# Performance work log

Hardware: AMD Instinct MI355X
Metric: run time of the kernel (lower is better)

The kernel has to match this reference:

```python
import jax, jax.numpy as jnp
import numpy as np

H = 1024
HEADS = 16
FFN = 4096
EPS = 1e-5


def _layernorm(x, g, b):
    mu = jnp.mean(x, axis=-1, keepdims=True)
    var = jnp.mean((x - mu) ** 2, axis=-1, keepdims=True)
    return (x - mu) * jax.lax.rsqrt(var + EPS) * g + b


def setup_inputs() -> dict:
    key = jax.random.key(0)
    ks = jax.random.split(key, 12)
    N, L = 2, 2048
    s = 1.0 / np.sqrt(H)
    inp = {
        "src_hidden": jax.random.normal(ks[0], (N, L, H), dtype=jnp.float32),
        "key_mask": jnp.ones((N, L), dtype=jnp.int32),
        "Wq": jax.random.normal(ks[1], (H, H), dtype=jnp.float32) * s,
        "bq": jnp.zeros((H,), dtype=jnp.float32),
        "Wk": jax.random.normal(ks[2], (H, H), dtype=jnp.float32) * s,
        "bk": jnp.zeros((H,), dtype=jnp.float32),
        "Wv": jax.random.normal(ks[3], (H, H), dtype=jnp.float32) * s,
        "bv": jnp.zeros((H,), dtype=jnp.float32),
        "Wo": jax.random.normal(ks[4], (H, H), dtype=jnp.float32) * s,
        "bo": jnp.zeros((H,), dtype=jnp.float32),
        "ln1_g": jnp.ones((H,), dtype=jnp.float32),
        "ln1_b": jnp.zeros((H,), dtype=jnp.float32),
        "W1": jax.random.normal(ks[5], (H, FFN), dtype=jnp.float32) * s,
        "b1": jnp.zeros((FFN,), dtype=jnp.float32),
        "W2": jax.random.normal(ks[6], (FFN, H), dtype=jnp.float32) * (1.0 / np.sqrt(FFN)),
        "b2": jnp.zeros((H,), dtype=jnp.float32),
        "ln2_g": jnp.ones((H,), dtype=jnp.float32),
        "ln2_b": jnp.zeros((H,), dtype=jnp.float32),
    }
    return inp


def reference(src_hidden, key_mask, Wq, bq, Wk, bk, Wv, bv, Wo, bo,
              ln1_g, ln1_b, W1, b1, W2, b2, ln2_g, ln2_b):
    N, L, _ = src_hidden.shape
    d = H // HEADS
    # projections -> (N, heads, L, d)
    q = (src_hidden @ Wq + bq).reshape(N, L, HEADS, d).transpose(0, 2, 1, 3)
    k = (src_hidden @ Wk + bk).reshape(N, L, HEADS, d).transpose(0, 2, 1, 3)
    v = (src_hidden @ Wv + bv).reshape(N, L, HEADS, d).transpose(0, 2, 1, 3)
    # faithful quirk: Q/=sqrt(H) and K/=sqrt(H)  =>  scores scaled by 1/H
    sims = jnp.einsum('bhid,bhjd->bhij', q, k) / H  # (N, heads, L, L)
    mask = key_mask[:, None, None, :] != 0          # (N,1,1,L), masked=False
    sims = jnp.where(mask, sims, -jnp.inf)
    attn = jax.nn.softmax(sims, axis=-1)
    ctx = jnp.einsum('bhij,bhjd->bhid', attn, v)
    concats = ctx.transpose(0, 2, 1, 3).reshape(N, L, H)
    mhsa = concats @ Wo + bo
    # residual + LN1
    x = _layernorm(mhsa + src_hidden, ln1_g, ln1_b)
    # FFN (dropout=0 / eval) + residual + LN2
    ffn = jax.nn.relu(x @ W1 + b1) @ W2 + b2
    out = _layernorm(ffn + x, ln2_g, ln2_b)
    return out
```

## Files before the change

kernel.cpp:

```cpp
#include <hip/hip_runtime.h>
#include <math.h>

#define Hd   1024
#define SEQL 2048
#define NB   2
#define NHEADS 16
#define FFND 4096
#define ROWS 4096
#define QKVLD 3072

typedef __attribute__((ext_vector_type(8))) short short8;
typedef __attribute__((ext_vector_type(4))) float f32x4;

__device__ __forceinline__ unsigned short f2bf(float f) {
  union { float f; unsigned int u; } v; v.f = f;
  return (unsigned short)((v.u + 0x7fffu + ((v.u >> 16) & 1u)) >> 16);
}
__device__ __forceinline__ unsigned short f2bf_fast(float f) {
  union { float f; unsigned int u; } v; v.f = f;
  return (unsigned short)((v.u + 0x8000u) >> 16);
}
__device__ __forceinline__ float bf2f(unsigned short u) {
  union { unsigned int u; float f; } v; v.u = (unsigned int)u << 16;
  return v.f;
}

__device__ __forceinline__ void gl_lds16(const unsigned short* g,
                                         unsigned short* l) {
  __builtin_amdgcn_global_load_lds(
      (const __attribute__((address_space(1))) void*)g,
      (__attribute__((address_space(3))) void*)l, 16, 0, 0);
}

__global__ __launch_bounds__(256) void convert_bf16(
    const float* __restrict__ in, unsigned short* __restrict__ out) {
  const int i = (blockIdx.x * 256 + threadIdx.x) * 4;
  float4 x = *(const float4*)&in[i];
  ushort4 o;
  o.x = f2bf(x.x); o.y = f2bf(x.y); o.z = f2bf(x.z); o.w = f2bf(x.w);
  *(ushort4*)&out[i] = o;
}

__global__ __launch_bounds__(256) void convert_transpose(
    const float* __restrict__ W, int ld,
    unsigned short* __restrict__ Wt, int ldt) {
  __shared__ float T[64][65];
  const int t = threadIdx.x;
  const int c0 = blockIdx.x * 64, r0 = blockIdx.y * 64;
#pragma unroll
  for (int p = 0; p < 4; ++p) {
    const int lin = t + p * 256;
    const int r = lin >> 4, c4 = (lin & 15) * 4;
    float4 x = *(const float4*)&W[(size_t)(r0 + r) * ld + c0 + c4];
    T[r][c4 + 0] = x.x; T[r][c4 + 1] = x.y;
    T[r][c4 + 2] = x.z; T[r][c4 + 3] = x.w;
  }
  __syncthreads();
#pragma unroll
  for (int p = 0; p < 2; ++p) {
    const int lin = t + p * 256;
    const int oc = lin >> 3, ch = (lin & 7) * 8;
    union { unsigned short u[8]; uint4 v; } x;
#pragma unroll
    for (int i = 0; i < 8; ++i) x.u[i] = f2bf(T[ch + i][oc]);
    *(uint4*)&Wt[(size_t)(c0 + oc) * ldt + r0 + ch] = x.v;
  }
}

__global__ __launch_bounds__(256) void convert_transpose4(
    const float* __restrict__ W0, const float* __restrict__ W1,
    const float* __restrict__ W2, const float* __restrict__ W3,
    unsigned short* __restrict__ T0, unsigned short* __restrict__ T1,
    unsigned short* __restrict__ T2, unsigned short* __restrict__ T3) {
  __shared__ float T[64][65];
  const float* W = (blockIdx.z == 0) ? W0 : (blockIdx.z == 1) ? W1
                 : (blockIdx.z == 2) ? W2 : W3;
  unsigned short* Wt = (blockIdx.z == 0) ? T0 : (blockIdx.z == 1) ? T1
                     : (blockIdx.z == 2) ? T2 : T3;
  const int t = threadIdx.x;
  const int c0 = blockIdx.x * 64, r0 = blockIdx.y * 64;
#pragma unroll
  for (int p = 0; p < 4; ++p) {
    const int lin = t + p * 256;
    const int r = lin >> 4, c4 = (lin & 15) * 4;
    float4 x = *(const float4*)&W[(size_t)(r0 + r) * Hd + c0 + c4];
    T[r][c4 + 0] = x.x; T[r][c4 + 1] = x.y;
    T[r][c4 + 2] = x.z; T[r][c4 + 3] = x.w;
  }
  __syncthreads();
#pragma unroll
  for (int p = 0; p < 2; ++p) {
    const int lin = t + p * 256;
    const int oc = lin >> 3, ch = (lin & 7) * 8;
    union { unsigned short u[8]; uint4 v; } x;
#pragma unroll
    for (int i = 0; i < 8; ++i) x.u[i] = f2bf(T[ch + i][oc]);
    *(uint4*)&Wt[(size_t)(c0 + oc) * Hd + r0 + ch] = x.v;
  }
}

__global__ __launch_bounds__(256) void concat3(
    const float* __restrict__ a, const float* __restrict__ b,
    const float* __restrict__ c, float* __restrict__ o) {
  const int i = blockIdx.x * 256 + threadIdx.x;
  o[i] = (i < 1024) ? a[i] : (i < 2048 ? b[i - 1024] : c[i - 2048]);
}

__global__ __launch_bounds__(256) void transpose_v(
    const unsigned short* __restrict__ v, unsigned short* __restrict__ vt) {
  __shared__ unsigned short T[64][72];
  const int t = threadIdx.x;
  const int s0 = (blockIdx.x & 31) * 64;
  const int bh = blockIdx.x >> 5;
  const int b = bh >> 4, h = bh & 15;
#pragma unroll
  for (int p = 0; p < 2; ++p) {
    const int lin = t + p * 256;
    const int r = lin >> 3, c8 = (lin & 7) * 8;
    *(uint4*)&T[r][c8] =
        *(const uint4*)&v[(size_t)(b * SEQL + s0 + r) * QKVLD + h * 64 + c8];
  }
  __syncthreads();
#pragma unroll
  for (int p = 0; p < 2; ++p) {
    const int lin = t + p * 256;
    const int d = lin >> 3, c8 = (lin & 7) * 8;
    union { unsigned short u[8]; uint4 v4; } x;
#pragma unroll
    for (int i = 0; i < 8; ++i) x.u[i] = T[c8 + i][d];
    *(uint4*)&vt[(size_t)(bh * 64 + d) * SEQL + s0 + c8] = x.v4;
  }
}

template <int BN, int MODE, int OUTBF>
__global__ __launch_bounds__(256, (BN == 128 ? 3 : 4)) void gemm_bt(
    const unsigned short* __restrict__ A, int lda,
    const unsigned short* __restrict__ Bt, int ldb,
    const float* __restrict__ bias,
    void* __restrict__ Cv, int ldc, int K) {
  constexpr int NI = (BN == 128) ? 4 : 2;
  __shared__ unsigned short As[128 * 32];
  __shared__ unsigned short Bs[BN * 32];
  const int t = threadIdx.x;
  const int wave = t >> 6, lane = t & 63;
  const int l16 = lane & 15, quad = lane >> 4;
  const int m0 = blockIdx.y * 128, n0 = blockIdx.x * BN;
  const int wm = (wave >> 1) * 64, wn = (wave & 1) * (BN / 2);
  const int srow = wave * 16 + (lane >> 2);
  const int scol = (lane & 3) * 8;

  f32x4 acc[4][NI];
#pragma unroll
  for (int i = 0; i < 4; ++i)
#pragma unroll
    for (int j = 0; j < NI; ++j) acc[i][j] = (f32x4){0.f, 0.f, 0.f, 0.f};

  const unsigned short* Ap0 = &A[(size_t)(m0 + srow) * lda + scol];
  const unsigned short* Ap1 = &A[(size_t)(m0 + 64 + srow) * lda + scol];
  const unsigned short* Bp0 = &Bt[(size_t)(n0 + srow) * ldb + scol];
  const unsigned short* Bp1 =
      (BN == 128) ? &Bt[(size_t)(n0 + 64 + srow) * ldb + scol] : Bp0;
  unsigned short* lA0 = &As[(wave * 16) * 32];
  unsigned short* lA1 = &As[(64 + wave * 16) * 32];
  unsigned short* lB0 = &Bs[(wave * 16) * 32];
  unsigned short* lB1 = (BN == 128) ? &Bs[(64 + wave * 16) * 32] : lB0;

  for (int k0 = 0; k0 < K; k0 += 32) {
    gl_lds16(Ap0 + k0, lA0);
    gl_lds16(Ap1 + k0, lA1);
    gl_lds16(Bp0 + k0, lB0);
    if (BN == 128) gl_lds16(Bp1 + k0, lB1);
    __syncthreads();

    short8 af[4], bfr[NI];
#pragma unroll
    for (int mi = 0; mi < 4; ++mi)
      af[mi] = *(const short8*)&As[(wm + mi * 16 + l16) * 32 + quad * 8];
#pragma unroll
    for (int ni = 0; ni < NI; ++ni)
      bfr[ni] = *(const short8*)&Bs[(wn + ni * 16 + l16) * 32 + quad * 8];
#pragma unroll
    for (int mi = 0; mi < 4; ++mi)
#pragma unroll
      for (int ni = 0; ni < NI; ++ni)
        acc[mi][ni] = __builtin_amdgcn_mfma_f32_16x16x32_bf16(
            af[mi], bfr[ni], acc[mi][ni], 0, 0, 0);
    __syncthreads();
  }

#pragma unroll
  for (int mi = 0; mi < 4; ++mi) {
#pragma unroll
    for (int ni = 0; ni < NI; ++ni) {
      const int col = n0 + wn + ni * 16 + l16;
      const float bv = (MODE == 2) ? 0.0f : bias[col];
#pragma unroll
      for (int r = 0; r < 4; ++r) {
        const int row = m0 + wm + mi * 16 + quad * 4 + r;
        float v = acc[mi][ni][r] + bv;
        if (MODE == 1) v = fmaxf(v, 0.0f);
        if (OUTBF) {
          ((unsigned short*)Cv)[(size_t)row * ldc + col] = f2bf_fast(v);
        } else {
          float* Cf = (float*)Cv;
          if (MODE == 2) Cf[(size_t)row * ldc + col] += v;
          else           Cf[(size_t)row * ldc + col] = v;
        }
      }
    }
  }
}

template <int MODE>
__global__ __launch_bounds__(512, 2) void gemm256(
    const unsigned short* __restrict__ A, int lda,
    const unsigned short* __restrict__ Bt, int ldb,
    const float* __restrict__ bias,
    unsigned short* __restrict__ C, int ldc, int K) {
  __shared__ unsigned short As[2][256 * 64];
  __shared__ unsigned short Bs[2][256 * 64];
  const int t = threadIdx.x;
  const int wave = t >> 6, lane = t & 63;
  const int l16 = lane & 15, quad = lane >> 4;
  const int m0 = blockIdx.y * 256, n0 = blockIdx.x * 256;
  const int wm = (wave >> 2) * 128, wn = (wave & 3) * 64;

  const int srow = t >> 3;
  const int scol = 8 * ((t & 7) ^ ((t >> 3) & 7));
  const unsigned short* Ab = &A[(size_t)(m0 + srow) * lda + scol];
  const unsigned short* Bb = &Bt[(size_t)(n0 + srow) * ldb + scol];

  auto stgA = [&](int buf, int kt, int h) {
    const unsigned short* g = Ab + (size_t)(h * 128) * lda + kt * 64;
    unsigned short* l = &As[buf][h * 8192 + wave * 512];
    gl_lds16(g, l);
    gl_lds16(g + (size_t)64 * lda, l + 4096);
  };
  auto stgB = [&](int buf, int kt, int h) {
    const unsigned short* g = Bb + (size_t)(h * 128) * ldb + kt * 64;
    unsigned short* l = &Bs[buf][h * 8192 + wave * 512];
    gl_lds16(g, l);
    gl_lds16(g + (size_t)64 * ldb, l + 4096);
  };

  f32x4 acc[8][4];
#pragma unroll
  for (int i = 0; i < 8; ++i)
#pragma unroll
    for (int j = 0; j < 4; ++j) acc[i][j] = (f32x4){0.f, 0.f, 0.f, 0.f};

  const int NT = K >> 6;

  stgA(0, 0, 0); stgA(0, 0, 1);
  stgB(0, 0, 0); stgB(0, 0, 1);
  if (NT > 1) {
    stgB(1, 1, 0); stgB(1, 1, 1);
    asm volatile("s_waitcnt vmcnt(4)" ::: "memory");
  } else {
    asm volatile("s_waitcnt vmcnt(0)" ::: "memory");
  }
  __builtin_amdgcn_s_barrier();

  short8 bq[4];
  for (int tk = 0; tk < NT; ++tk) {
    const int cb = tk & 1, nb = cb ^ 1;
    short8 af[4];

#pragma unroll
    for (int mi = 0; mi < 4; ++mi) {
      const int r = wm + mi * 16 + l16;
      af[mi] = *(const short8*)&As[cb][r * 64 + ((quad * 8) ^ ((r & 7) * 8))];
    }
#pragma unroll
    for (int ni = 0; ni < 4; ++ni) {
      const int r = wn + ni * 16 + l16;
      bq[ni] = *(const short8*)&Bs[cb][r * 64 + ((quad * 8) ^ ((r & 7) * 8))];
    }
    if (tk + 1 < NT) stgA(nb, tk + 1, 0);
    __builtin_amdgcn_sched_barrier(0);
    __builtin_amdgcn_s_barrier();
    asm volatile("s_waitcnt lgkmcnt(0)" ::: "memory");
    __builtin_amdgcn_sched_barrier(0);
    __builtin_amdgcn_s_setprio(1);
#pragma unroll
    for (int mi = 0; mi < 4; ++mi)
#pragma unroll
      for (int ni = 0; ni < 4; ++ni)
        acc[mi][ni] = __builtin_amdgcn_mfma_f32_16x16x32_bf16(
            af[mi], bq[ni], acc[mi][ni], 0, 0, 0);
    __builtin_amdgcn_s_setprio(0);
    __builtin_amdgcn_s_barrier();

#pragma unroll
    for (int mi = 0; mi < 4; ++mi) {
      const int r = wm + 64 + mi * 16 + l16;
      af[mi] = *(const short8*)&As[cb][r * 64 + ((quad * 8) ^ ((r & 7) * 8))];
    }
    if (tk + 1 < NT) stgA(nb, tk + 1, 1);
    __builtin_amdgcn_sched_barrier(0);
    __builtin_amdgcn_s_barrier();
    asm volatile("s_waitcnt lgkmcnt(0)" ::: "memory");
    __builtin_amdgcn_sched_barrier(0);
    __builtin_amdgcn_s_setprio(1);
#pragma unroll
    for (int mi = 0; mi < 4; ++mi)
#pragma unroll
      for (int ni = 0; ni < 4; ++ni)
        acc[4 + mi][ni] = __builtin_amdgcn_mfma_f32_16x16x32_bf16(
            af[mi], bq[ni], acc[4 + mi][ni], 0, 0, 0);
    __builtin_amdgcn_s_setprio(0);
    __builtin_amdgcn_s_barrier();

#pragma unroll
    for (int mi = 0; mi < 4; ++mi) {
      const int r = wm + mi * 16 + l16;
      af[mi] = *(const short8*)&As[cb][r * 64 + ((32 + quad * 8) ^ ((r & 7) * 8))];
    }
#pragma unroll
    for (int ni = 0; ni < 4; ++ni) {
      const int r = wn + ni * 16 + l16;
      bq[ni] = *(const short8*)&Bs[cb][r * 64 + ((32 + quad * 8) ^ ((r & 7) * 8))];
    }
    __builtin_amdgcn_sched_barrier(0);
    __builtin_amdgcn_s_barrier();
    asm volatile("s_waitcnt lgkmcnt(0)" ::: "memory");
    __builtin_amdgcn_sched_barrier(0);
    __builtin_amdgcn_s_setprio(1);
#pragma unroll
    for (int mi = 0; mi < 4; ++mi)
#pragma unroll
      for (int ni = 0; ni < 4; ++ni)
        acc[mi][ni] = __builtin_amdgcn_mfma_f32_16x16x32_bf16(
            af[mi], bq[ni], acc[mi][ni], 0, 0, 0);
    __builtin_amdgcn_s_setprio(0);
    __builtin_amdgcn_s_barrier();

#pragma unroll
    for (int mi = 0; mi < 4; ++mi) {
      const int r = wm + 64 + mi * 16 + l16;
      af[mi] = *(const short8*)&As[cb][r * 64 + ((32 + quad * 8) ^ ((r & 7) * 8))];
    }
    if (tk + 2 < NT) { stgB(cb, tk + 2, 0); stgB(cb, tk + 2, 1); }
    __builtin_amdgcn_sched_barrier(0);
    __builtin_amdgcn_s_barrier();
    asm volatile("s_waitcnt lgkmcnt(0)" ::: "memory");
    __builtin_amdgcn_sched_barrier(0);
    __builtin_amdgcn_s_setprio(1);
#pragma unroll
    for (int mi = 0; mi < 4; ++mi)
#pragma unroll
      for (int ni = 0; ni < 4; ++ni)
        acc[4 + mi][ni] = __builtin_amdgcn_mfma_f32_16x16x32_bf16(
            af[mi], bq[ni], acc[4 + mi][ni], 0, 0, 0);
    __builtin_amdgcn_s_setprio(0);
    if (tk + 2 < NT) {
      asm volatile("s_waitcnt vmcnt(4)" ::: "memory");
    } else if (tk + 1 < NT) {
      asm volatile("s_waitcnt vmcnt(0)" ::: "memory");
    }
    __builtin_amdgcn_s_barrier();
  }

#pragma unroll
  for (int mi = 0; mi < 8; ++mi) {
#pragma unroll
    for (int ni = 0; ni < 4; ++ni) {
      const int col = n0 + wn + ni * 16 + l16;
      const float bv = bias[col];
#pragma unroll
      for (int r = 0; r < 4; ++r) {
        const int row = m0 + wm + mi * 16 + quad * 4 + r;
        float v = acc[mi][ni][r] + bv;
        if (MODE == 1) v = fmaxf(v, 0.0f);
        C[(size_t)row * ldc + col] = f2bf_fast(v);
      }
    }
  }
}

__global__ __launch_bounds__(256, 5) void attn_mfma(
    const unsigned short* __restrict__ Q,
    const unsigned short* __restrict__ K,
    const unsigned short* __restrict__ Vt,
    const int* __restrict__ mask,
    unsigned short* __restrict__ Op,
    float* __restrict__ ls) {
  __shared__ unsigned short Qs[64 * 72];
  __shared__ unsigned short Ks[64 * 72];
  __shared__ unsigned short Vs[64 * 72];
  unsigned short* Ps = Qs;

  const int t = threadIdx.x;
  const int wave = t >> 6, lane = t & 63;
  const int l16 = lane & 15, quad = lane >> 4;
  const int qb = blockIdx.x & 31;
  const int h  = (blockIdx.x >> 5) & 15;
  const int b  = (blockIdx.x >> 9) & 1;
  const int jh = blockIdx.x >> 10;
  const int q0 = qb * 64;
  const int bh = b * NHEADS + h;
  const int jbeg = jh * (SEQL / 2), jend = jbeg + SEQL / 2;
  const float NEGINF = -__builtin_inff();

  const int lr = t >> 3, lc8 = (t & 7) * 8;
  const unsigned short* Kbase = &K[(size_t)(b * SEQL + lr) * QKVLD + h * 64 + lc8];
  const unsigned short* Vbase = &Vt[(size_t)(bh * 64 + lr) * SEQL + lc8];
  const size_t Krow32 = (size_t)32 * QKVLD;

#pragma unroll
  for (int p = 0; p < 2; ++p) {
    const int r = lr + p * 32;
    *(uint4*)&Qs[r * 72 + lc8] =
        *(const uint4*)&Q[(size_t)(b * SEQL + q0 + r) * QKVLD + h * 64 + lc8];
  }
  __syncthreads();
  const short8 aq0 = *(const short8*)&Qs[(wave * 16 + l16) * 72 + quad * 8];
  const short8 aq1 = *(const short8*)&Qs[(wave * 16 + l16) * 72 + 32 + quad * 8];

  float lrow[4] = {0.f, 0.f, 0.f, 0.f};
  f32x4 accO[4];
#pragma unroll
  for (int nd = 0; nd < 4; ++nd) accO[nd] = (f32x4){0.f, 0.f, 0.f, 0.f};

  uint4 kv0 = *(const uint4*)(Kbase + (size_t)jbeg * QKVLD);
  uint4 kv1 = *(const uint4*)(Kbase + (size_t)jbeg * QKVLD + Krow32);
  uint4 vv0 = *(const uint4*)(Vbase + jbeg);
  uint4 vv1 = *(const uint4*)(Vbase + jbeg + 32 * SEQL);

  for (int j0 = jbeg; j0 < jend; j0 += 64) {
    __syncthreads();
    *(uint4*)&Ks[lr * 72 + lc8] = kv0;
    *(uint4*)&Ks[(lr + 32) * 72 + lc8] = kv1;
    *(uint4*)&Vs[lr * 72 + lc8] = vv0;
    *(uint4*)&Vs[(lr + 32) * 72 + lc8] = vv1;
    __syncthreads();

    if (j0 + 64 < jend) {
      const unsigned short* kp = Kbase + (size_t)(j0 + 64) * QKVLD;
      const unsigned short* vp = Vbase + (j0 + 64);
      kv0 = *(const uint4*)(kp);
      kv1 = *(const uint4*)(kp + Krow32);
      vv0 = *(const uint4*)(vp);
      vv1 = *(const uint4*)(vp + 32 * SEQL);
    }

#pragma unroll
    for (int nt = 0; nt < 4; ++nt) {
      short8 bk0 = *(const short8*)&Ks[(nt * 16 + l16) * 72 + quad * 8];
      short8 bk1 = *(const short8*)&Ks[(nt * 16 + l16) * 72 + 32 + quad * 8];
      f32x4 z = (f32x4){0.f, 0.f, 0.f, 0.f};
      z = __builtin_amdgcn_mfma_f32_16x16x32_bf16(aq0, bk0, z, 0, 0, 0);
      z = __builtin_amdgcn_mfma_f32_16x16x32_bf16(aq1, bk1, z, 0, 0, 0);
      const bool ok = mask[b * SEQL + j0 + nt * 16 + l16] != 0;
      unsigned short pk[4];
#pragma unroll
      for (int r = 0; r < 4; ++r) {
        const float x = ok ? z[r] * (1.0f / 1024.0f) : NEGINF;
        const float p = __expf(x);
        lrow[r] += p;
        pk[r] = f2bf_fast(p);
      }
#pragma unroll
      for (int r = 0; r < 4; ++r)
        Ps[(wave * 16 + quad * 4 + r) * 72 + nt * 16 + l16] = pk[r];
    }

    short8 ap0 = *(const short8*)&Ps[(wave * 16 + l16) * 72 + quad * 8];
    short8 ap1 = *(const short8*)&Ps[(wave * 16 + l16) * 72 + 32 + quad * 8];
#pragma unroll
    for (int nd = 0; nd < 4; ++nd) {
      short8 bv0 = *(const short8*)&Vs[(nd * 16 + l16) * 72 + quad * 8];
      short8 bv1 = *(const short8*)&Vs[(nd * 16 + l16) * 72 + 32 + quad * 8];
      accO[nd] = __builtin_amdgcn_mfma_f32_16x16x32_bf16(ap0, bv0, accO[nd], 0, 0, 0);
      accO[nd] = __builtin_amdgcn_mfma_f32_16x16x32_bf16(ap1, bv1, accO[nd], 0, 0, 0);
    }
  }

#pragma unroll
  for (int r = 0; r < 4; ++r) {
#pragma unroll
    for (int off = 1; off < 16; off <<= 1)
      lrow[r] += __shfl_xor(lrow[r], off, 64);
  }
  if (l16 == 0) {
#pragma unroll
    for (int r = 0; r < 4; ++r)
      ls[((size_t)(jh * NB + b) * NHEADS + h) * SEQL + q0 + wave * 16 +
         quad * 4 + r] = lrow[r];
  }
#pragma unroll
  for (int nd = 0; nd < 4; ++nd)
#pragma unroll
    for (int r = 0; r < 4; ++r) {
      const int rowg = b * SEQL + q0 + wave * 16 + quad * 4 + r;
      Op[(size_t)jh * ROWS * Hd + (size_t)rowg * Hd + h * 64 + nd * 16 + l16] =
          f2bf_fast(accO[nd][r]);
    }
}

__global__ __launch_bounds__(256) void attn_combine(
    const unsigned short* __restrict__ Op, const float* __restrict__ ls,
    unsigned short* __restrict__ ctxb) {
  const int row = blockIdx.x;
  const int b = row >> 11, q = row & (SEQL - 1);
  const int t = threadIdx.x;
  const int c0 = t * 4, h = t >> 4;
  const float l0 = ls[((size_t)(b)*NHEADS + h) * SEQL + q];
  const float l1 = ls[((size_t)(NB + b) * NHEADS + h) * SEQL + q];
  const float inv = 1.0f / (l0 + l1);
  ushort4 a = *(const ushort4*)&Op[(size_t)row * Hd + c0];
  ushort4 c = *(const ushort4*)&Op[(size_t)ROWS * Hd + (size_t)row * Hd + c0];
  ushort4 o;
  o.x = f2bf_fast((bf2f(a.x) + bf2f(c.x)) * inv);
  o.y = f2bf_fast((bf2f(a.y) + bf2f(c.y)) * inv);
  o.z = f2bf_fast((bf2f(a.z) + bf2f(c.z)) * inv);
  o.w = f2bf_fast((bf2f(a.w) + bf2f(c.w)) * inv);
  *(ushort4*)&ctxb[(size_t)row * Hd + c0] = o;
}

template <int ABF>
__global__ __launch_bounds__(256) void add_ln_kernel(
    const void* Av, const float* R,
    const float* __restrict__ gamma, const float* __restrict__ beta,
    float* out, unsigned short* outb) {
  const int row = blockIdx.x;
  const int t = threadIdx.x;
  const size_t baser = (size_t)row * Hd;

  float a0, a1, a2, a3;
  if (ABF) {
    ushort4 a = *(const ushort4*)&((const unsigned short*)Av)[baser + t * 4];
    a0 = bf2f(a.x); a1 = bf2f(a.y); a2 = bf2f(a.z); a3 = bf2f(a.w);
  } else {
    float4 a = *(const float4*)&((const float*)Av)[baser + t * 4];
    a0 = a.x; a1 = a.y; a2 = a.z; a3 = a.w;
  }
  float4 r = *(const float4*)&R[baser + t * 4];
  float x0 = a0 + r.x, x1 = a1 + r.y, x2 = a2 + r.z, x3 = a3 + r.w;
  float s  = x0 + x1 + x2 + x3;
  float ss = x0 * x0 + x1 * x1 + x2 * x2 + x3 * x3;

#pragma unroll
  for (int off = 32; off > 0; off >>= 1) {
    s  += __shfl_down(s, off, 64);
    ss += __shfl_down(ss, off, 64);
  }

  __shared__ float rs[4], rss[4];
  __shared__ float sh_mean, sh_rstd;
  if ((t & 63) == 0) { rs[t >> 6] = s; rss[t >> 6] = ss; }
  __syncthreads();
  if (t == 0) {
    const float S  = rs[0] + rs[1] + rs[2] + rs[3];
    const float SS = rss[0] + rss[1] + rss[2] + rss[3];
    const float mean = S * (1.0f / Hd);
    const float var  = SS * (1.0f / Hd) - mean * mean;
    sh_mean = mean;
    sh_rstd = rsqrtf(var + 1e-5f);
  }
  __syncthreads();
  const float mean = sh_mean, rstd = sh_rstd;

  float4 gm = *(const float4*)&gamma[t * 4];
  float4 bt = *(const float4*)&beta[t * 4];
  float4 o;
  o.x = (x0 - mean) * rstd * gm.x + bt.x;
  o.y = (x1 - mean) * rstd * gm.y + bt.y;
  o.z = (x2 - mean) * rstd * gm.z + bt.z;
  o.w = (x3 - mean) * rstd * gm.w + bt.w;
  *(float4*)&out[baser + t * 4] = o;
  if (outb) {
    ushort4 ob;
    ob.x = f2bf(o.x); ob.y = f2bf(o.y); ob.z = f2bf(o.z); ob.w = f2bf(o.w);
    *(ushort4*)&outb[baser + t * 4] = ob;
  }
}

extern "C" void kernel_launch(void* const* d_in, const int* in_sizes, int n_in,
                              void* d_out, int out_size, void* d_ws, size_t ws_size,
                              hipStream_t stream) {
  const float* src  = (const float*)d_in[0];
  const int*   kmsk = (const int*)  d_in[1];
  const float* Wq   = (const float*)d_in[2];
  const float* bq   = (const float*)d_in[3];
  const float* Wk   = (const float*)d_in[4];
  const float* bk   = (const float*)d_in[5];
  const float* Wv   = (const float*)d_in[6];
  const float* bv   = (const float*)d_in[7];
  const float* Wo   = (const float*)d_in[8];
  const float* bo   = (const float*)d_in[9];
  const float* ln1g = (const float*)d_in[10];
  const float* ln1b = (const float*)d_in[11];
  const float* W1   = (const float*)d_in[12];
  const float* b1   = (const float*)d_in[13];
  const float* W2   = (const float*)d_in[14];
  const float* b2   = (const float*)d_in[15];
  const float* ln2g = (const float*)d_in[16];
  const float* ln2b = (const float*)d_in[17];

  char* w8 = (char*)d_ws;
  char* o8 = (char*)d_out;
  const size_t MB = 1024 * 1024;
  unsigned short* srcb  = (unsigned short*)(w8 + 0 * MB);
  unsigned short* WqkvT = (unsigned short*)(w8 + 8 * MB);
  float*          bqkv  = (float*)(w8 + 14 * MB);
  unsigned short* qkv   = (unsigned short*)(w8 + 16 * MB);
  unsigned short* vt    = (unsigned short*)(w8 + 40 * MB);
  unsigned short* Opart = (unsigned short*)(w8 + 0 * MB);
  float*          ls    = (float*)(o8 + 8 * MB);
  unsigned short* WoT   = (unsigned short*)(o8 + 9 * MB);
  unsigned short* ctxb  = (unsigned short*)d_out;
  float*          mhsa  = (float*)(w8 + 16 * MB);
  float*          x1    = (float*)d_out;
  unsigned short* x1b   = (unsigned short*)(w8 + 8 * MB);
  unsigned short* W1T   = (unsigned short*)(w8 + 0 * MB);
  unsigned short* hb    = (unsigned short*)(w8 + 16 * MB);
  unsigned short* W2T   = (unsigned short*)(w8 + 0 * MB);
  unsigned short* f2b   = (unsigned short*)(w8 + 8 * MB);

  dim3 blk(256);
  dim3 blk8(512);

  convert_bf16<<<ROWS * Hd / 1024, blk, 0, stream>>>(src, srcb);
  convert_transpose4<<<dim3(16, 16, 4), blk, 0, stream>>>(
      Wq, Wk, Wv, Wo, WqkvT, WqkvT + 1024 * 1024, WqkvT + 2 * 1024 * 1024, WoT);
  concat3<<<12, blk, 0, stream>>>(bq, bk, bv, bqkv);

  gemm256<0><<<dim3(QKVLD / 256, ROWS / 256), blk8, 0, stream>>>(
      srcb, Hd, WqkvT, Hd, bqkv, qkv, QKVLD, Hd);

  transpose_v<<<1024, blk, 0, stream>>>(qkv + 2048, vt);
  attn_mfma<<<2048, blk, 0, stream>>>(qkv, qkv + 1024, vt, kmsk, Opart, ls);
  attn_combine<<<ROWS, blk, 0, stream>>>(Opart, ls, ctxb);

  gemm_bt<64, 0, 0><<<dim3(Hd / 64, ROWS / 128), blk, 0, stream>>>(
      ctxb, Hd, WoT, Hd, bo, mhsa, Hd, Hd);

  add_ln_kernel<0><<<ROWS, blk, 0, stream>>>(mhsa, src, ln1g, ln1b, x1, x1b);

  convert_transpose<<<dim3(64, 16), blk, 0, stream>>>(W1, FFND, W1T, Hd);
  gemm256<1><<<dim3(FFND / 256, ROWS / 256), blk8, 0, stream>>>(
      x1b, Hd, W1T, Hd, b1, hb, FFND, Hd);
  convert_transpose<<<dim3(16, 64), blk, 0, stream>>>(W2, Hd, W2T, FFND);
  gemm_bt<64, 0, 1><<<dim3(Hd / 64, ROWS / 128), blk, 0, stream>>>(
      hb, FFND, W2T, FFND, b2, f2b, Hd, FFND);

  add_ln_kernel<1><<<ROWS, blk, 0, stream>>>(f2b, x1, ln2g, ln2b,
                                             (float*)d_out, nullptr);
}
```

Baseline: 404.2 us.

## Relax GEMM sync fences and streamline attention softmax and LDS use

In the GEMM main loop, the sched_barrier pairs and explicit lgkmcnt(0) waits around each block barrier are removed, leaving only s_barrier, so the compiler can schedule LDS reads and MFMAs freely. In the attention kernel, Q fragments are loaded straight from global memory instead of being staged through LDS, and P gets its own LDS buffer. The exponent now uses a raw v_exp_f32 on a fused scale-plus-mask-bias FMA, with log2(e) folded into the constant. P is written to LDS with a row permutation, matched on the read side, intended to cut bank conflicts, and s_setprio is placed around the MFMA sections. The risks are that the compiler's own scheduling may be worse than the hand-placed fences, and the extra P buffer raises LDS use per block, which can lower occupancy.

```diff
diff --git a/kernel.cpp b/kernel.cpp
--- a/kernel.cpp
+++ b/kernel.cpp
@@ -277,10 +277,7 @@
       bq[ni] = *(const short8*)&Bs[cb][r * 64 + ((quad * 8) ^ ((r & 7) * 8))];
     }
     if (tk + 1 < NT) stgA(nb, tk + 1, 0);
-    __builtin_amdgcn_sched_barrier(0);
-    __builtin_amdgcn_s_barrier();
-    asm volatile("s_waitcnt lgkmcnt(0)" ::: "memory");
-    __builtin_amdgcn_sched_barrier(0);
+    __builtin_amdgcn_s_barrier();
     __builtin_amdgcn_s_setprio(1);
 #pragma unroll
     for (int mi = 0; mi < 4; ++mi)
@@ -297,10 +294,7 @@
       af[mi] = *(const short8*)&As[cb][r * 64 + ((quad * 8) ^ ((r & 7) * 8))];
     }
     if (tk + 1 < NT) stgA(nb, tk + 1, 1);
-    __builtin_amdgcn_sched_barrier(0);
-    __builtin_amdgcn_s_barrier();
-    asm volatile("s_waitcnt lgkmcnt(0)" ::: "memory");
-    __builtin_amdgcn_sched_barrier(0);
+    __builtin_amdgcn_s_barrier();
     __builtin_amdgcn_s_setprio(1);
 #pragma unroll
     for (int mi = 0; mi < 4; ++mi)
@@ -321,10 +315,7 @@
       const int r = wn + ni * 16 + l16;
       bq[ni] = *(const short8*)&Bs[cb][r * 64 + ((32 + quad * 8) ^ ((r & 7) * 8))];
     }
-    __builtin_amdgcn_sched_barrier(0);
-    __builtin_amdgcn_s_barrier();
-    asm volatile("s_waitcnt lgkmcnt(0)" ::: "memory");
-    __builtin_amdgcn_sched_barrier(0);
+    __builtin_amdgcn_s_barrier();
     __builtin_amdgcn_s_setprio(1);
 #pragma unroll
     for (int mi = 0; mi < 4; ++mi)
@@ -341,10 +332,7 @@
       af[mi] = *(const short8*)&As[cb][r * 64 + ((32 + quad * 8) ^ ((r & 7) * 8))];
     }
     if (tk + 2 < NT) { stgB(cb, tk + 2, 0); stgB(cb, tk + 2, 1); }
-    __builtin_amdgcn_sched_barrier(0);
-    __builtin_amdgcn_s_barrier();
-    asm volatile("s_waitcnt lgkmcnt(0)" ::: "memory");
-    __builtin_amdgcn_sched_barrier(0);
+    __builtin_amdgcn_s_barrier();
     __builtin_amdgcn_s_setprio(1);
 #pragma unroll
     for (int mi = 0; mi < 4; ++mi)
@@ -385,10 +373,9 @@
     const int* __restrict__ mask,
     unsigned short* __restrict__ Op,
     float* __restrict__ ls) {
-  __shared__ unsigned short Qs[64 * 72];
   __shared__ unsigned short Ks[64 * 72];
   __shared__ unsigned short Vs[64 * 72];
-  unsigned short* Ps = Qs;
+  __shared__ unsigned short Ps[64 * 72];
 
   const int t = threadIdx.x;
   const int wave = t >> 6, lane = t & 63;
@@ -401,21 +388,19 @@
   const int bh = b * NHEADS + h;
   const int jbeg = jh * (SEQL / 2), jend = jbeg + SEQL / 2;
   const float NEGINF = -__builtin_inff();
+  const float C2 = 1.4426950408889634f * (1.0f / 1024.0f);
 
   const int lr = t >> 3, lc8 = (t & 7) * 8;
   const unsigned short* Kbase = &K[(size_t)(b * SEQL + lr) * QKVLD + h * 64 + lc8];
   const unsigned short* Vbase = &Vt[(size_t)(bh * 64 + lr) * SEQL + lc8];
   const size_t Krow32 = (size_t)32 * QKVLD;
 
-#pragma unroll
-  for (int p = 0; p < 2; ++p) {
-    const int r = lr + p * 32;
-    *(uint4*)&Qs[r * 72 + lc8] =
-        *(const uint4*)&Q[(size_t)(b * SEQL + q0 + r) * QKVLD + h * 64 + lc8];
-  }
-  __syncthreads();
-  const short8 aq0 = *(const short8*)&Qs[(wave * 16 + l16) * 72 + quad * 8];
-  const short8 aq1 = *(const short8*)&Qs[(wave * 16 + l16) * 72 + 32 + quad * 8];
+  const unsigned short* Qrow =
+      &Q[(size_t)(b * SEQL + q0 + wave * 16 + l16) * QKVLD + h * 64];
+  const short8 aq0 = *(const short8*)&Qrow[quad * 8];
+  const short8 aq1 = *(const short8*)&Qrow[32 + quad * 8];
+
+  const int prow_rd = wave * 16 + 2 * (l16 >> 2) + (l16 & 1) + 8 * ((l16 >> 1) & 1);
 
   float lrow[4] = {0.f, 0.f, 0.f, 0.f};
   f32x4 accO[4];
@@ -449,24 +434,26 @@
       short8 bk0 = *(const short8*)&Ks[(nt * 16 + l16) * 72 + quad * 8];
       short8 bk1 = *(const short8*)&Ks[(nt * 16 + l16) * 72 + 32 + quad * 8];
       f32x4 z = (f32x4){0.f, 0.f, 0.f, 0.f};
+      __builtin_amdgcn_s_setprio(1);
       z = __builtin_amdgcn_mfma_f32_16x16x32_bf16(aq0, bk0, z, 0, 0, 0);
       z = __builtin_amdgcn_mfma_f32_16x16x32_bf16(aq1, bk1, z, 0, 0, 0);
-      const bool ok = mask[b * SEQL + j0 + nt * 16 + l16] != 0;
-      unsigned short pk[4];
+      __builtin_amdgcn_s_setprio(0);
+      const float mb =
+          (mask[b * SEQL + j0 + nt * 16 + l16] != 0) ? 0.0f : NEGINF;
 #pragma unroll
       for (int r = 0; r < 4; ++r) {
-        const float x = ok ? z[r] * (1.0f / 1024.0f) : NEGINF;
-        const float p = __expf(x);
+        const float xx = fmaf(z[r], C2, mb);
+        float p;
+        asm("v_exp_f32 %0, %1" : "=v"(p) : "v"(xx));
         lrow[r] += p;
-        pk[r] = f2bf_fast(p);
+        Ps[(wave * 16 + 2 * quad + (r & 1) + 8 * (r >> 1)) * 72 +
+           nt * 16 + l16] = f2bf_fast(p);
       }
-#pragma unroll
-      for (int r = 0; r < 4; ++r)
-        Ps[(wave * 16 + quad * 4 + r) * 72 + nt * 16 + l16] = pk[r];
-    }
-
-    short8 ap0 = *(const short8*)&Ps[(wave * 16 + l16) * 72 + quad * 8];
-    short8 ap1 = *(const short8*)&Ps[(wave * 16 + l16) * 72 + 32 + quad * 8];
+    }
+
+    short8 ap0 = *(const short8*)&Ps[prow_rd * 72 + quad * 8];
+    short8 ap1 = *(const short8*)&Ps[prow_rd * 72 + 32 + quad * 8];
+    __builtin_amdgcn_s_setprio(1);
 #pragma unroll
     for (int nd = 0; nd < 4; ++nd) {
       short8 bv0 = *(const short8*)&Vs[(nd * 16 + l16) * 72 + quad * 8];
@@ -474,6 +461,7 @@
       accO[nd] = __builtin_amdgcn_mfma_f32_16x16x32_bf16(ap0, bv0, accO[nd], 0, 0, 0);
       accO[nd] = __builtin_amdgcn_mfma_f32_16x16x32_bf16(ap1, bv1, accO[nd], 0, 0, 0);
     }
+    __builtin_amdgcn_s_setprio(0);
   }
 
 #pragma unroll
```

New measurement: 411.9 us. Within noise of the previous version (+1.9%).
